# Performance work log

Measured on AMD Instinct MI355X. Metric: run time of the kernel, lower is better.

The kernel has to match this reference:

```python
import jax, jax.numpy as jnp
import numpy as np

N = 50000        # nodes
E = 800000       # directed edges
NUM_E = 10000    # hyperedges
NFEAT, NHID, NOUT = 256, 128, 64
K = 10
TEMP = 5.0


def gcn_prop(h, src, dst, n):
    # PyG GCNConv propagation with added self-loops: D^-1/2 (A+I) D^-1/2 h
    ew = jnp.ones(src.shape[0], h.dtype)
    deg = 1.0 + jax.ops.segment_sum(ew, dst, num_segments=n)  # self-loop adds 1
    dinv = jax.lax.rsqrt(deg)
    norm = dinv[src] * dinv[dst]                   # [E]
    out = jax.ops.segment_sum(h[src] * norm[:, None], dst, num_segments=n)
    out = out + h / deg[:, None]                   # self-loop term (weight deg^-1)
    return out


def gcn_conv(x, W, b, src, dst, n):
    return gcn_prop(x @ W, src, dst, n) + b


def hgnnp_conv(x, W, b, hv, he, n, num_e):
    # dhg HGNNPConv: theta(x) then v->e mean aggregation, then e->v mean
    h = x @ W + b
    ones = jnp.ones(hv.shape[0], h.dtype)
    e_deg = jnp.maximum(jax.ops.segment_sum(ones, he, num_segments=num_e), 1.0)
    v_deg = jnp.maximum(jax.ops.segment_sum(ones, hv, num_segments=n), 1.0)
    e_feat = jax.ops.segment_sum(h[hv], he, num_segments=num_e) / e_deg[:, None]
    v_out = jax.ops.segment_sum(e_feat[he], hv, num_segments=n) / v_deg[:, None]
    return v_out


def setup_inputs() -> dict:
    key = jax.random.key(0)
    ks = jax.random.split(key, 12)
    x = jax.random.normal(ks[0], (N, NFEAT), jnp.float32)
    edge_index = jax.random.randint(ks[1], (2, E), 0, N)
    hv_idx = jax.random.randint(ks[2], (200000,), 0, N)
    he_idx = jax.random.randint(ks[3], (200000,), 0, NUM_E)

    def glorot(k, shape):
        lim = float(np.sqrt(6.0 / (shape[0] + shape[1])))
        return jax.random.uniform(k, shape, jnp.float32, -lim, lim)

    return {
        "x": x, "edge_index": edge_index, "hv_idx": hv_idx, "he_idx": he_idx,
        "gcn_W1": glorot(ks[4], (NFEAT, NHID)), "gcn_b1": jnp.zeros((NHID,), jnp.float32),
        "gcn_W2": glorot(ks[5], (NHID, NOUT)), "gcn_b2": jnp.zeros((NOUT,), jnp.float32),
        "hg_W1": glorot(ks[6], (NFEAT, NHID)), "hg_b1": jnp.zeros((NHID,), jnp.float32),
        "hg_W2": glorot(ks[7], (NHID, NOUT)), "hg_b2": jnp.zeros((NOUT,), jnp.float32),
        "num_iter": 1,
    }


def reference(x, edge_index, hv_idx, he_idx,
              gcn_W1, gcn_b1, gcn_W2, gcn_b2,
              hg_W1, hg_b1, hg_W2, hg_b2, num_iter):
    src, dst = edge_index[0], edge_index[1]

    # HGNNP_GCN encoder (dropout is identity in eval-style reference)
    x1 = jax.nn.relu(gcn_conv(x, gcn_W1, gcn_b1, src, dst, N))
    x2 = gcn_conv(x1, gcn_W2, gcn_b2, src, dst, N)
    x3 = jax.nn.relu(hgnnp_conv(x, hg_W1, hg_b1, hv_idx, he_idx, N, NUM_E))
    x4 = hgnnp_conv(x3, hg_W2, hg_b2, hv_idx, he_idx, N, NUM_E)  # is_last: no act
    embeds = x2 * 0.5 + x4 * 0.5                     # [N, NOUT]

    # row-normalize (diag(1/||row||) @ data)
    data = embeds / jnp.linalg.norm(embeds, axis=1, keepdims=True)

    # kmeans++ init is a host-side, data-dependent pick; use deterministic
    # strided row selection from the (detached) normalized embeddings.
    init_idx = jnp.arange(K) * (N // K)
    mu = jax.lax.stop_gradient(data[init_idx])       # [K, NOUT]

    for _ in range(int(num_iter)):
        dist = data @ mu.T                           # [N, K]
        r = jax.nn.softmax(TEMP * dist, axis=1)
        cluster_r = r.sum(axis=0)                    # [K]
        cluster_mean = r.T @ data                    # [K, NOUT]
        mu = cluster_mean / cluster_r[:, None]

    dist = data @ mu.T
    r = jax.nn.softmax(TEMP * dist, axis=1)
    return mu, r, embeds, dist
```

## Files before the change

### kernel.cpp

```cpp
#include <hip/hip_runtime.h>
#include <hip/hip_bf16.h>


#define NN   50000
#define NP   50048
#define EE   800000
#define NINC 200000
#define NEH  10000
#define KCL  10

#define MU_OFF  0
#define R_OFF   640
#define EMB_OFF 500640
#define D_OFF   3700640

typedef __hip_bfloat16 bf16;
typedef unsigned short u16;
typedef unsigned int   u32;
typedef __attribute__((ext_vector_type(8))) short short8;
typedef __attribute__((ext_vector_type(4))) float f32x4;

__device__ __forceinline__ float b2f(bf16 v){ return __bfloat162float(v); }
__device__ __forceinline__ float us2f(u16 u){ return __uint_as_float(((unsigned)u) << 16); }
__device__ __forceinline__ u16 f2bu(float f){
  unsigned u = __float_as_uint(f);
  return (u16)((u + 0x7fffu + ((u >> 16) & 1u)) >> 16);
}
__device__ __forceinline__ bf16 f2b(float f){
  u16 r = f2bu(f);
  bf16 h;
  reinterpret_cast<u16&>(h) = r;
  return h;
}
__device__ __forceinline__ float ldf(const void* p, size_t i, int isbf){
  return isbf ? b2f(((const bf16*)p)[i]) : ((const float*)p)[i];
}
__device__ __forceinline__ void stf(void* p, size_t i, float v, int isbf){
  if (isbf) ((bf16*)p)[i] = f2b(v);
  else      ((float*)p)[i] = v;
}

__global__ void k_detect(const u16* __restrict__ xr, int* flag){
  __shared__ int bad;
  if (threadIdx.x == 0) bad = 0;
  __syncthreads();
  for (int i = threadIdx.x; i < 4096; i += 256){
    int e = (xr[i] >> 7) & 0xFF;
    if (e >= 0xEF) bad = 1;
  }
  __syncthreads();
  if (threadIdx.x == 0) *flag = bad ? 0 : 1;
}

__global__ void k_aconv(const void* __restrict__ x, u16* __restrict__ xb,
                        const int* __restrict__ flag){
  int i = blockIdx.x*256 + threadIdx.x;
  const int n4 = NN*256/4;
  if (i >= n4) return;
  ushort4 o;
  if (flag[0]){
    o = ((const ushort4*)x)[i];
  } else {
    float4 v = ((const float4*)x)[i];
    o = make_ushort4(f2bu(v.x), f2bu(v.y), f2bu(v.z), f2bu(v.w));
  }
  ((ushort4*)xb)[i] = o;
}

__global__ void k_wprep(const void* gW1, const void* hW1, const void* gW2, const void* hW2,
                        const void* gb1, const void* hb1, const void* gb2, const void* hb2,
                        u16* gW1t, u16* hW1t, u16* gW2t, u16* hW2t,
                        float* gb1f, float* hb1f, float* gb2f, float* hb2f,
                        const int* __restrict__ flag){
  const int isbf = flag[0];
  int i = blockIdx.x*256 + threadIdx.x;
  if (i < 256*128){
    int n = i >> 8, k = i & 255;
    gW1t[i] = f2bu(ldf(gW1, (size_t)k*128 + n, isbf));
    hW1t[i] = f2bu(ldf(hW1, (size_t)k*128 + n, isbf));
  }
  if (i < 64*128){
    int n = i >> 7, k = i & 127;
    gW2t[i] = f2bu(ldf(gW2, (size_t)k*64 + n, isbf));
    hW2t[i] = f2bu(ldf(hW2, (size_t)k*64 + n, isbf));
  }
  if (i < 128){ gb1f[i] = ldf(gb1,i,isbf); hb1f[i] = ldf(hb1,i,isbf); }
  if (i < 64) { gb2f[i] = ldf(gb2,i,isbf); hb2f[i] = ldf(hb2,i,isbf); }
}

template<int NBKT, int NPB>
__global__ __launch_bounds__(256) void k_histA(const int* __restrict__ key,
                                               int* __restrict__ HA, int chunk){
  __shared__ u32 hist[NBKT];
  for (int i = threadIdx.x; i < NBKT; i += 256) hist[i] = 0;
  __syncthreads();
  int base = blockIdx.x*chunk;
  for (int i = threadIdx.x; i < chunk; i += 256)
    atomicAdd(&hist[key[base+i]/NPB], 1u);
  __syncthreads();
  int* out = HA + blockIdx.x*NBKT;
  for (int i = threadIdx.x; i < NBKT; i += 256) out[i] = (int)hist[i];
}

__global__ void k_scanA_all(int* HAg, int* HAv, int* HAe,
                            int* bsg, int* bsv, int* bse){
  int* HA; int* bs; int nch;
  if (blockIdx.x == 0){ HA = HAg; bs = bsg; nch = 128; }
  else if (blockIdx.x == 1){ HA = HAv; bs = bsv; nch = 64; }
  else { HA = HAe; bs = bse; nch = 64; }
  __shared__ int s[256];
  int t = threadIdx.x;
  int run = 0;
  if (t < 250){
    for (int c = 0; c < nch; ++c){
      int v = HA[c*250 + t];
      HA[c*250 + t] = run;
      run += v;
    }
  }
  int own = (t < 250) ? run : 0;
  s[t] = own; __syncthreads();
  #pragma unroll
  for (int off = 1; off < 256; off <<= 1){
    int add = (t >= off) ? s[t-off] : 0;
    __syncthreads();
    s[t] += add;
    __syncthreads();
  }
  if (t < 250) bs[t] = s[t] - own;
  if (t == 255) bs[250] = s[255];
}

template<int NBKT, int NPB>
__global__ __launch_bounds__(256) void k_fillA(const int* __restrict__ key,
    const int* __restrict__ val, const int* __restrict__ HA,
    const int* __restrict__ bs, u32* __restrict__ packed, int chunk){
  __shared__ u32 cur[NBKT];
  const int* pre = HA + blockIdx.x*NBKT;
  for (int i = threadIdx.x; i < NBKT; i += 256) cur[i] = (u32)(bs[i] + pre[i]);
  __syncthreads();
  int base = blockIdx.x*chunk;
  for (int i = threadIdx.x; i < chunk; i += 256){
    int k = key[base+i];
    int b = k / NPB;
    u32 pos = atomicAdd(&cur[b], 1u);
    packed[pos] = ((u32)(k - b*NPB) << 16) | (u32)val[base+i];
  }
}

template<int NPB>
__global__ __launch_bounds__(256) void k_fillB(const u32* __restrict__ packed,
    const int* __restrict__ bs, int* __restrict__ csr,
    int* __restrict__ cnt, int* __restrict__ rp){
  __shared__ u32 hist[NPB];
  __shared__ int s[256];
  __shared__ u32 cur[NPB];
  const int b = blockIdx.x;
  const int s0 = bs[b], m = bs[b+1] - s0;
  const int t = threadIdx.x;
  for (int i = t; i < NPB; i += 256) hist[i] = 0;
  __syncthreads();
  for (int i = t; i < m; i += 256)
    atomicAdd(&hist[packed[s0+i] >> 16], 1u);
  __syncthreads();
  int own = (t < NPB) ? (int)hist[t] : 0;
  s[t] = own; __syncthreads();
  #pragma unroll
  for (int off = 1; off < 256; off <<= 1){
    int add = (t >= off) ? s[t-off] : 0;
    __syncthreads();
    s[t] += add;
    __syncthreads();
  }
  if (t < NPB){
    int excl = s[t] - own;
    cnt[b*NPB + t] = own;
    rp[b*NPB + t]  = s0 + excl;
    cur[t] = (u32)(s0 + excl);
  }
  __syncthreads();
  for (int i = t; i < m; i += 256){
    u32 p = packed[s0+i];
    u32 pos = atomicAdd(&cur[p >> 16], 1u);
    csr[pos] = (int)(p & 0xffffu);
  }
}

__global__ void k_invs(const int* __restrict__ cg, const int* __restrict__ cv,
                       const int* __restrict__ ce,
                       float* dinv, float* invv, float* inve){
  int i = blockIdx.x*256 + threadIdx.x;
  if (i < NN){
    float d = 1.0f + (float)cg[i];
    dinv[i] = rsqrtf(d);
    invv[i] = 1.0f / fmaxf((float)cv[i], 1.0f);
  } else if (i < NP){
    dinv[i] = 0.f;
  }
  if (i < NEH) inve[i] = 1.0f / fmaxf((float)ce[i], 1.0f);
}

template<int KDIM, int NCOL>
__global__ __launch_bounds__(256) void k_gemm_mfma(
    const u16* __restrict__ A, const u16* __restrict__ Wt,
    const float* __restrict__ bias, const float* __restrict__ rowscale,
    u16* __restrict__ C, int relu)
{
  constexpr int NT  = NCOL/16;
  constexpr int LDA = 40;
  __shared__ __align__(16) u16 Asl[64][LDA];
  __shared__ __align__(16) u16 Wsl[NCOL][LDA];
  const int tid  = threadIdx.x;
  const int wave = tid >> 6, lane = tid & 63;
  const int l15 = lane & 15, l4 = lane >> 4;
  const int row0 = blockIdx.x * 64;
  const int ar = tid >> 2, aq = tid & 3;
  constexpr int NW = NCOL*4/256;

  f32x4 acc[NT] = {};

  for (int kk = 0; kk < KDIM; kk += 32){
    {
      uint4 v = *(const uint4*)(A + (size_t)(row0 + ar)*KDIM + kk + aq*8);
      *(uint4*)&Asl[ar][aq*8] = v;
    }
    #pragma unroll
    for (int w2 = 0; w2 < NW; ++w2){
      int c = tid + w2*256;
      int n = c >> 2, q = c & 3;
      uint4 v = *(const uint4*)(Wt + (size_t)n*KDIM + kk + q*8);
      *(uint4*)&Wsl[n][q*8] = v;
    }
    __syncthreads();
    short8 af = *(const short8*)&Asl[wave*16 + l15][l4*8];
    #pragma unroll
    for (int t = 0; t < NT; ++t){
      short8 bf = *(const short8*)&Wsl[t*16 + l15][l4*8];
      acc[t] = __builtin_amdgcn_mfma_f32_16x16x32_bf16(af, bf, acc[t], 0, 0, 0);
    }
    __syncthreads();
  }

  #pragma unroll
  for (int t = 0; t < NT; ++t){
    int gcol = t*16 + l15;
    float b = bias ? bias[gcol] : 0.f;
    #pragma unroll
    for (int e = 0; e < 4; ++e){
      int grow = row0 + wave*16 + l4*4 + e;
      float v = acc[t][e] + b;
      if (relu) v = fmaxf(v, 0.f);
      if (rowscale) v *= rowscale[grow];
      C[(size_t)grow*NCOL + gcol] = f2bu(v);
    }
  }
}

template<int F, bool OUTBF, bool SELF>
__global__ __launch_bounds__(256) void k_gather(
    const int* __restrict__ rp, const int* __restrict__ cnt,
    const int* __restrict__ csr, const float* __restrict__ scale,
    const u16* __restrict__ h, const float* __restrict__ bias,
    void* __restrict__ out, int relu)
{
  const int wave = threadIdx.x >> 6, lane = threadIdx.x & 63;
  const int d = blockIdx.x*4 + wave;
  const int k0 = rp[d], n = cnt[d];

  if constexpr (F == 128){
    const uint* h32 = (const uint*)h;
    float a0=0,a1=0,b0=0,b1=0,c0=0,c1=0,e0=0,e1=0;
    if (SELF){
      uint v = h32[(size_t)d*64 + lane];
      a0 = us2f((u16)v); a1 = us2f((u16)(v>>16));
    }
    for (int base = 0; base < n; base += 64){
      int mm = n - base; if (mm > 64) mm = 64;
      int idx = (lane < mm) ? csr[k0 + base + lane] : 0;
      int jj = 0;
      for (; jj + 4 <= mm; jj += 4){
        int s0=__shfl(idx,jj), s1=__shfl(idx,jj+1), s2=__shfl(idx,jj+2), s3=__shfl(idx,jj+3);
        uint v0 = h32[(size_t)s0*64 + lane];
        uint v1 = h32[(size_t)s1*64 + lane];
        uint v2 = h32[(size_t)s2*64 + lane];
        uint v3 = h32[(size_t)s3*64 + lane];
        a0 += us2f((u16)v0); a1 += us2f((u16)(v0>>16));
        b0 += us2f((u16)v1); b1 += us2f((u16)(v1>>16));
        c0 += us2f((u16)v2); c1 += us2f((u16)(v2>>16));
        e0 += us2f((u16)v3); e1 += us2f((u16)(v3>>16));
      }
      for (; jj < mm; ++jj){
        int s = __shfl(idx, jj);
        uint v = h32[(size_t)s*64 + lane];
        a0 += us2f((u16)v); a1 += us2f((u16)(v>>16));
      }
    }
    float sc = scale[d];
    float o0 = ((a0+b0)+(c0+e0))*sc;
    float o1 = ((a1+b1)+(c1+e1))*sc;
    if (bias){ o0 += bias[lane*2]; o1 += bias[lane*2+1]; }
    if (relu){ o0 = fmaxf(o0,0.f); o1 = fmaxf(o1,0.f); }
    if (OUTBF){
      ((uint*)out)[(size_t)d*64 + lane] = (uint)f2bu(o0) | ((uint)f2bu(o1) << 16);
    } else {
      ((float2*)out)[(size_t)d*64 + lane] = make_float2(o0, o1);
    }
  } else {
    float a=0,b=0,c=0,e=0;
    if (SELF) a = us2f(h[(size_t)d*64 + lane]);
    for (int base = 0; base < n; base += 64){
      int mm = n - base; if (mm > 64) mm = 64;
      int idx = (lane < mm) ? csr[k0 + base + lane] : 0;
      int jj = 0;
      for (; jj + 4 <= mm; jj += 4){
        int s0=__shfl(idx,jj), s1=__shfl(idx,jj+1), s2=__shfl(idx,jj+2), s3=__shfl(idx,jj+3);
        a += us2f(h[(size_t)s0*64 + lane]);
        b += us2f(h[(size_t)s1*64 + lane]);
        c += us2f(h[(size_t)s2*64 + lane]);
        e += us2f(h[(size_t)s3*64 + lane]);
      }
      for (; jj < mm; ++jj){
        int s = __shfl(idx, jj);
        a += us2f(h[(size_t)s*64 + lane]);
      }
    }
    float o = ((a+b)+(c+e))*scale[d];
    if (bias) o += bias[lane];
    if (relu) o = fmaxf(o, 0.f);
    if (OUTBF) ((u16*)out)[(size_t)d*64 + lane] = f2bu(o);
    else       ((float*)out)[(size_t)d*64 + lane] = o;
  }
}

__global__ void k_embeds(const float* __restrict__ x2, const float* __restrict__ x4,
                         void* __restrict__ out, float* __restrict__ data,
                         const int* __restrict__ flag){
  int row  = blockIdx.x*4 + (threadIdx.x >> 6);
  int lane = threadIdx.x & 63;
  if (row >= NN) return;
  size_t idx = (size_t)row*64 + lane;
  float v = 0.5f*(x2[idx] + x4[idx]);
  float ss = v*v;
  #pragma unroll
  for (int off=32; off>0; off>>=1) ss += __shfl_xor(ss, off);
  float inv = rsqrtf(ss);
  data[idx] = v*inv;
  stf(out, EMB_OFF + idx, v, flag[0]);
}

__global__ void k_mu_init(const float* __restrict__ data, float* __restrict__ mu){
  int p = blockIdx.x*256 + threadIdx.x;
  if (p >= KCL*64) return;
  int k = p >> 6, f = p & 63;
  mu[p] = data[(size_t)k*(NN/KCL)*64 + f];
}

__global__ __launch_bounds__(128) void k_cluster_accum(const float* __restrict__ data,
    const float* __restrict__ mu, float* csum, float* cr, const int* nit, int iter)
{
  if (iter >= nit[0]) return;
  __shared__ float dt[128][65];
  __shared__ float rl[128][KCL];
  __shared__ float ms[KCL*64];
  int tid = threadIdx.x;
  int rowbase = blockIdx.x*128;
  for (int j=tid; j<KCL*64; j+=128) ms[j] = mu[j];
  for (int j=tid; j<128*64; j+=128){
    int rr = j>>6, f = j&63;
    int row = rowbase + rr;
    dt[rr][f] = (row<NN) ? data[(size_t)row*64+f] : 0.f;
  }
  __syncthreads();
  {
    int row = rowbase + tid;
    float dot[KCL];
    #pragma unroll
    for (int k2=0;k2<KCL;k2++) dot[k2]=0.f;
    for (int f=0; f<64; f++){
      float a = dt[tid][f];
      #pragma unroll
      for (int k2=0;k2<KCL;k2++) dot[k2] = fmaf(a, ms[k2*64+f], dot[k2]);
    }
    float m = -1e30f;
    #pragma unroll
    for (int k2=0;k2<KCL;k2++) m = fmaxf(m, 5.0f*dot[k2]);
    float s = 0.f, ev[KCL];
    #pragma unroll
    for (int k2=0;k2<KCL;k2++){ ev[k2] = expf(5.0f*dot[k2]-m); s += ev[k2]; }
    float inv = 1.0f/s;
    #pragma unroll
    for (int k2=0;k2<KCL;k2++) rl[tid][k2] = (row<NN) ? ev[k2]*inv : 0.f;
  }
  __syncthreads();
  for (int p=tid; p<KCL*64; p+=128){
    int k2 = p>>6, f = p&63;
    float acc = 0.f;
    for (int r2=0;r2<128;r2++) acc += rl[r2][k2]*dt[r2][f];
    unsafeAtomicAdd(&csum[p], acc);
  }
  if (tid < KCL){
    float acc = 0.f;
    for (int r2=0;r2<128;r2++) acc += rl[r2][tid];
    unsafeAtomicAdd(&cr[tid], acc);
  }
}

__global__ void k_mu_update(float* mu, float* csum, float* cr, const int* nit, int iter){
  if (iter >= nit[0]) return;
  int p = threadIdx.x;
  float c = csum[p];
  float r = cr[p>>6];
  __syncthreads();
  mu[p] = c / r;
  csum[p] = 0.f;
  if (p < KCL) cr[p] = 0.f;
}

__global__ __launch_bounds__(128) void k_cluster_final(const float* __restrict__ data,
    const float* __restrict__ mu, void* __restrict__ out, const int* __restrict__ flag)
{
  __shared__ float dt[128][65];
  __shared__ float ms[KCL*64];
  int tid = threadIdx.x;
  int rowbase = blockIdx.x*128;
  for (int j=tid; j<KCL*64; j+=128) ms[j] = mu[j];
  for (int j=tid; j<128*64; j+=128){
    int rr = j>>6, f = j&63;
    int row = rowbase + rr;
    dt[rr][f] = (row<NN) ? data[(size_t)row*64+f] : 0.f;
  }
  __syncthreads();
  int row = rowbase + tid;
  if (row >= NN) return;
  int isbf = flag[0];
  float dot[KCL];
  #pragma unroll
  for (int k2=0;k2<KCL;k2++) dot[k2]=0.f;
  for (int f=0; f<64; f++){
    float a = dt[tid][f];
    #pragma unroll
    for (int k2=0;k2<KCL;k2++) dot[k2] = fmaf(a, ms[k2*64+f], dot[k2]);
  }
  float m = -1e30f;
  #pragma unroll
  for (int k2=0;k2<KCL;k2++) m = fmaxf(m, 5.0f*dot[k2]);
  float s = 0.f, ev[KCL];
  #pragma unroll
  for (int k2=0;k2<KCL;k2++){ ev[k2] = expf(5.0f*dot[k2]-m); s += ev[k2]; }
  float inv = 1.0f/s;
  #pragma unroll
  for (int k2=0;k2<KCL;k2++){
    stf(out, (size_t)D_OFF + (size_t)row*KCL + k2, dot[k2],     isbf);
    stf(out, (size_t)R_OFF + (size_t)row*KCL + k2, ev[k2]*inv,  isbf);
  }
}

__global__ void k_mu_out(const float* __restrict__ mu, void* __restrict__ out,
                         const int* __restrict__ flag){
  int p = blockIdx.x*256 + threadIdx.x;
  if (p < KCL*64) stf(out, MU_OFF + p, mu[p], flag[0]);
}

extern "C" void kernel_launch(void* const* d_in, const int* in_sizes, int n_in,
                              void* d_out, int out_size, void* d_ws, size_t ws_size,
                              hipStream_t stream)
{
  const void* x   = d_in[0];
  const int*  ei  = (const int*)d_in[1];
  const int*  hv  = (const int*)d_in[2];
  const int*  he  = (const int*)d_in[3];
  const void* gW1 = d_in[4];
  const void* gb1 = d_in[5];
  const void* gW2 = d_in[6];
  const void* gb2 = d_in[7];
  const void* hW1 = d_in[8];
  const void* hb1 = d_in[9];
  const void* hW2 = d_in[10];
  const void* hb2 = d_in[11];
  const int*  nit = (const int*)d_in[12];

  float* ws = (float*)d_ws;
  size_t o = 0;
  u16*   xb  = (u16*)(ws + o); o += (size_t)NP*128;
  u16*   BAb = (u16*)(ws + o); o += (size_t)NP*64;
  u16*   BBb = (u16*)(ws + o); o += (size_t)NP*64;
  u16*   BCb = (u16*)(ws + o); o += (size_t)NP*64;
  u16*   BDb = (u16*)(ws + o); o += (size_t)NEH*64;
  u16*  gW1t = (u16*)(ws + o); o += 16384;
  u16*  hW1t = (u16*)(ws + o); o += 16384;
  u16*  gW2t = (u16*)(ws + o); o += 4096;
  u16*  hW2t = (u16*)(ws + o); o += 4096;
  float* gb1f = ws + o; o += 128;
  float* hb1f = ws + o; o += 128;
  float* gb2f = ws + o; o += 64;
  float* hb2f = ws + o; o += 64;
  float* dinv = ws + o; o += 50048;
  float* invv = ws + o; o += 50048;
  float* inve = ws + o; o += 10048;
  float* mu   = ws + o; o += 640;
  float* csum = ws + o; o += 640;
  float* cr   = ws + o; o += 64;
  int*   dflg = (int*)(ws + o); o += 16;
  float* x2f   = (float*)xb;
  float* x4f   = (float*)xb + (size_t)NP*64;
  float* dataf = (float*)BBb;
  int* ib = (int*)(ws + o);
  size_t io = 0;
  int* cg    = ib + io; io += NN;
  int* cv    = ib + io; io += NN;
  int* ce    = ib + io; io += NEH + 48;
  int* rp_g  = ib + io; io += NN;
  int* rp_v  = ib + io; io += NN;
  int* rp_e  = ib + io; io += NEH + 48;
  int* csr_g = ib + io; io += EE;
  int* csr_e = ib + io; io += NINC;
  int* csr_v = ib + io; io += NINC;
  int* HAg   = ib + io; io += 128*250;
  int* HAv   = ib + io; io += 64*250;
  int* HAe   = ib + io; io += 64*250;
  int* bsg   = ib + io; io += 256;
  int* bsv   = ib + io; io += 256;
  int* bse   = ib + io; io += 256;
  u32* pg = (u32*)(ib + io); io += EE;
  u32* pv = (u32*)(ib + io); io += NINC;
  u32* pe = (u32*)(ib + io); io += NINC;

  const int* srcp = ei;
  const int* dstp = ei + EE;
  dim3 B(256);
  const int NBP = (NP + 255)/256;

  k_detect<<<dim3(1), B, 0, stream>>>((const u16*)x, dflg);
  k_aconv<<<dim3(12500), B, 0, stream>>>(x, xb, dflg);
  k_wprep<<<dim3(128), B, 0, stream>>>(gW1, hW1, gW2, hW2, gb1, hb1, gb2, hb2,
                                       gW1t, hW1t, gW2t, hW2t,
                                       gb1f, hb1f, gb2f, hb2f, dflg);

  k_histA<250,200><<<dim3(128), B, 0, stream>>>(dstp, HAg, 6250);
  k_histA<250,200><<<dim3(64),  B, 0, stream>>>(hv,   HAv, 3125);
  k_histA<250, 40><<<dim3(64),  B, 0, stream>>>(he,   HAe, 3125);
  k_scanA_all<<<dim3(3), B, 0, stream>>>(HAg, HAv, HAe, bsg, bsv, bse);
  k_fillA<250,200><<<dim3(128), B, 0, stream>>>(dstp, srcp, HAg, bsg, pg, 6250);
  k_fillA<250,200><<<dim3(64),  B, 0, stream>>>(hv,   he,   HAv, bsv, pv, 3125);
  k_fillA<250, 40><<<dim3(64),  B, 0, stream>>>(he,   hv,   HAe, bse, pe, 3125);
  k_fillB<200><<<dim3(250), B, 0, stream>>>(pg, bsg, csr_g, cg, rp_g);
  k_fillB<200><<<dim3(250), B, 0, stream>>>(pv, bsv, csr_v, cv, rp_v);
  k_fillB< 40><<<dim3(250), B, 0, stream>>>(pe, bse, csr_e, ce, rp_e);
  k_invs<<<dim3(NBP), B, 0, stream>>>(cg, cv, ce, dinv, invv, inve);

  const int NB = NP/64;
  k_gemm_mfma<256,128><<<dim3(NB), B, 0, stream>>>(xb, gW1t, nullptr, dinv, BAb, 0);
  k_gather<128,true,true><<<dim3(NN/4), B, 0, stream>>>(rp_g, cg, csr_g, dinv,
                                                        BAb, gb1f, BBb, 1);
  k_gemm_mfma<256,128><<<dim3(NB), B, 0, stream>>>(xb, hW1t, hb1f, nullptr, BAb, 0);
  k_gather<128,true,false><<<dim3(NEH/4), B, 0, stream>>>(rp_e, ce, csr_e, inve,
                                                          BAb, nullptr, BDb, 0);
  k_gather<128,true,false><<<dim3(NN/4), B, 0, stream>>>(rp_v, cv, csr_v, invv,
                                                         BDb, nullptr, BCb, 1);
  k_gemm_mfma<128,64><<<dim3(NB), B, 0, stream>>>(BBb, gW2t, nullptr, dinv, BAb, 0);
  k_gather<64,false,true><<<dim3(NN/4), B, 0, stream>>>(rp_g, cg, csr_g, dinv,
                                                        BAb, gb2f, x2f, 0);
  k_gemm_mfma<128,64><<<dim3(NB), B, 0, stream>>>(BCb, hW2t, hb2f, nullptr, BAb, 0);
  k_gather<64,true,false><<<dim3(NEH/4), B, 0, stream>>>(rp_e, ce, csr_e, inve,
                                                         BAb, nullptr, BDb, 0);
  k_gather<64,false,false><<<dim3(NN/4), B, 0, stream>>>(rp_v, cv, csr_v, invv,
                                                         BDb, nullptr, x4f, 0);

  k_embeds<<<dim3((NN+3)/4), B, 0, stream>>>(x2f, x4f, d_out, dataf, dflg);

  k_mu_init<<<dim3(3), B, 0, stream>>>(dataf, mu);
  hipMemsetAsync(csum, 0, (640+64)*4, stream);
  const int CB = (NN + 127)/128;
  for (int it = 0; it < 4; ++it){
    k_cluster_accum<<<dim3(CB), dim3(128), 0, stream>>>(dataf, mu, csum, cr, nit, it);
    k_mu_update    <<<dim3(1),  dim3(640), 0, stream>>>(mu, csum, cr, nit, it);
  }
  k_cluster_final<<<dim3(CB), dim3(128), 0, stream>>>(dataf, mu, d_out, dflg);
  k_mu_out       <<<dim3(3),  B, 0, stream>>>(mu, d_out, dflg);
}
```

Before: 380.5 us.

## Replace atomic cluster accumulation with per-block partials and deterministic reduction

The k-means accumulation kernel is restructured to 200 blocks of 640 threads, each handling 250 rows. Each block writes per-block partial sums, and a separate single-block kernel reduces them, replacing global float atomics and the memset. Row dot products now read data directly with float4 loads instead of staging it in shared memory, and the final kernel uses 256-thread blocks. The goal is to remove atomic contention and the per-block shared-memory staging, at the cost of an extra kernel launch per iteration and a serial 200-way reduction.

```diff
diff --git a/kernel.cpp b/kernel.cpp
--- a/kernel.cpp
+++ b/kernel.cpp
@@ -355,103 +355,112 @@
   mu[p] = data[(size_t)k*(NN/KCL)*64 + f];
 }
 
-__global__ __launch_bounds__(128) void k_cluster_accum(const float* __restrict__ data,
-    const float* __restrict__ mu, float* csum, float* cr, const int* nit, int iter)
+__global__ __launch_bounds__(640) void k_cluster_iter(const float* __restrict__ data,
+    const float* __restrict__ mu, float* __restrict__ part, float* __restrict__ pcr,
+    const int* __restrict__ nit, int iter)
 {
   if (iter >= nit[0]) return;
-  __shared__ float dt[128][65];
-  __shared__ float rl[128][KCL];
-  __shared__ float ms[KCL*64];
-  int tid = threadIdx.x;
-  int rowbase = blockIdx.x*128;
-  for (int j=tid; j<KCL*64; j+=128) ms[j] = mu[j];
-  for (int j=tid; j<128*64; j+=128){
-    int rr = j>>6, f = j&63;
-    int row = rowbase + rr;
-    dt[rr][f] = (row<NN) ? data[(size_t)row*64+f] : 0.f;
-  }
-  __syncthreads();
-  {
-    int row = rowbase + tid;
+  __shared__ float ms[640];
+  __shared__ float rl[250][KCL];
+  const int tid = threadIdx.x;
+  ms[tid] = mu[tid];
+  __syncthreads();
+  const int r0 = blockIdx.x*250;
+  if (tid < 250){
+    const float4* dr = (const float4*)(data + (size_t)(r0 + tid)*64);
     float dot[KCL];
     #pragma unroll
-    for (int k2=0;k2<KCL;k2++) dot[k2]=0.f;
-    for (int f=0; f<64; f++){
-      float a = dt[tid][f];
+    for (int k=0;k<KCL;k++) dot[k]=0.f;
+    #pragma unroll
+    for (int q=0;q<16;q++){
+      float4 v = dr[q];
       #pragma unroll
-      for (int k2=0;k2<KCL;k2++) dot[k2] = fmaf(a, ms[k2*64+f], dot[k2]);
+      for (int k=0;k<KCL;k++){
+        float4 m4 = *(const float4*)&ms[k*64+q*4];
+        dot[k] = fmaf(v.x,m4.x,fmaf(v.y,m4.y,fmaf(v.z,m4.z,fmaf(v.w,m4.w,dot[k]))));
+      }
     }
     float m = -1e30f;
     #pragma unroll
-    for (int k2=0;k2<KCL;k2++) m = fmaxf(m, 5.0f*dot[k2]);
+    for (int k=0;k<KCL;k++) m = fmaxf(m, 5.0f*dot[k]);
     float s = 0.f, ev[KCL];
     #pragma unroll
-    for (int k2=0;k2<KCL;k2++){ ev[k2] = expf(5.0f*dot[k2]-m); s += ev[k2]; }
+    for (int k=0;k<KCL;k++){ ev[k] = expf(5.0f*dot[k]-m); s += ev[k]; }
     float inv = 1.0f/s;
     #pragma unroll
-    for (int k2=0;k2<KCL;k2++) rl[tid][k2] = (row<NN) ? ev[k2]*inv : 0.f;
-  }
-  __syncthreads();
-  for (int p=tid; p<KCL*64; p+=128){
-    int k2 = p>>6, f = p&63;
-    float acc = 0.f;
-    for (int r2=0;r2<128;r2++) acc += rl[r2][k2]*dt[r2][f];
-    unsafeAtomicAdd(&csum[p], acc);
-  }
-  if (tid < KCL){
-    float acc = 0.f;
-    for (int r2=0;r2<128;r2++) acc += rl[r2][tid];
-    unsafeAtomicAdd(&cr[tid], acc);
-  }
-}
-
-__global__ void k_mu_update(float* mu, float* csum, float* cr, const int* nit, int iter){
+    for (int k=0;k<KCL;k++) rl[tid][k] = ev[k]*inv;
+  }
+  __syncthreads();
+  const int w = tid >> 6, f = tid & 63;
+  float acc = 0.f, crp = 0.f;
+  for (int t = 0; t < 250; ++t){
+    float rv = rl[t][w];
+    acc = fmaf(rv, data[(size_t)(r0+t)*64 + f], acc);
+    crp += rv;
+  }
+  part[(size_t)blockIdx.x*640 + tid] = acc;
+  if (f == 0) pcr[blockIdx.x*16 + w] = crp;
+}
+
+__global__ void k_creduce(const float* __restrict__ part, const float* __restrict__ pcr,
+                          float* __restrict__ csum, float* __restrict__ cr,
+                          const int* __restrict__ nit, int iter){
   if (iter >= nit[0]) return;
   int p = threadIdx.x;
-  float c = csum[p];
-  float r = cr[p>>6];
-  __syncthreads();
-  mu[p] = c / r;
-  csum[p] = 0.f;
-  if (p < KCL) cr[p] = 0.f;
-}
-
-__global__ __launch_bounds__(128) void k_cluster_final(const float* __restrict__ data,
+  if (p < 640){
+    float a = 0.f;
+    for (int b = 0; b < 200; ++b) a += part[(size_t)b*640 + p];
+    csum[p] = a;
+  } else if (p < 640 + KCL){
+    int k = p - 640;
+    float a = 0.f;
+    for (int b = 0; b < 200; ++b) a += pcr[b*16 + k];
+    cr[k] = a;
+  }
+}
+
+__global__ void k_mu_update(float* __restrict__ mu, const float* __restrict__ csum,
+                            const float* __restrict__ cr,
+                            const int* __restrict__ nit, int iter){
+  if (iter >= nit[0]) return;
+  int p = threadIdx.x;
+  mu[p] = csum[p] / cr[p >> 6];
+}
+
+__global__ __launch_bounds__(256) void k_cluster_final(const float* __restrict__ data,
     const float* __restrict__ mu, void* __restrict__ out, const int* __restrict__ flag)
 {
-  __shared__ float dt[128][65];
-  __shared__ float ms[KCL*64];
-  int tid = threadIdx.x;
-  int rowbase = blockIdx.x*128;
-  for (int j=tid; j<KCL*64; j+=128) ms[j] = mu[j];
-  for (int j=tid; j<128*64; j+=128){
-    int rr = j>>6, f = j&63;
-    int row = rowbase + rr;
-    dt[rr][f] = (row<NN) ? data[(size_t)row*64+f] : 0.f;
-  }
-  __syncthreads();
-  int row = rowbase + tid;
+  __shared__ float ms[640];
+  const int tid = threadIdx.x;
+  for (int j = tid; j < 640; j += 256) ms[j] = mu[j];
+  __syncthreads();
+  int row = blockIdx.x*256 + tid;
   if (row >= NN) return;
-  int isbf = flag[0];
+  const int isbf = flag[0];
+  const float4* dr = (const float4*)(data + (size_t)row*64);
   float dot[KCL];
   #pragma unroll
-  for (int k2=0;k2<KCL;k2++) dot[k2]=0.f;
-  for (int f=0; f<64; f++){
-    float a = dt[tid][f];
-    #pragma unroll
-    for (int k2=0;k2<KCL;k2++) dot[k2] = fmaf(a, ms[k2*64+f], dot[k2]);
+  for (int k=0;k<KCL;k++) dot[k]=0.f;
+  #pragma unroll
+  for (int q=0;q<16;q++){
+    float4 v = dr[q];
+    #pragma unroll
+    for (int k=0;k<KCL;k++){
+      float4 m4 = *(const float4*)&ms[k*64+q*4];
+      dot[k] = fmaf(v.x,m4.x,fmaf(v.y,m4.y,fmaf(v.z,m4.z,fmaf(v.w,m4.w,dot[k]))));
+    }
   }
   float m = -1e30f;
   #pragma unroll
-  for (int k2=0;k2<KCL;k2++) m = fmaxf(m, 5.0f*dot[k2]);
+  for (int k=0;k<KCL;k++) m = fmaxf(m, 5.0f*dot[k]);
   float s = 0.f, ev[KCL];
   #pragma unroll
-  for (int k2=0;k2<KCL;k2++){ ev[k2] = expf(5.0f*dot[k2]-m); s += ev[k2]; }
+  for (int k=0;k<KCL;k++){ ev[k] = expf(5.0f*dot[k]-m); s += ev[k]; }
   float inv = 1.0f/s;
   #pragma unroll
-  for (int k2=0;k2<KCL;k2++){
-    stf(out, (size_t)D_OFF + (size_t)row*KCL + k2, dot[k2],     isbf);
-    stf(out, (size_t)R_OFF + (size_t)row*KCL + k2, ev[k2]*inv,  isbf);
+  for (int k=0;k<KCL;k++){
+    stf(out, (size_t)D_OFF + (size_t)row*KCL + k, dot[k],    isbf);
+    stf(out, (size_t)R_OFF + (size_t)row*KCL + k, ev[k]*inv, isbf);
   }
 }
 
@@ -500,6 +509,8 @@
   float* mu   = ws + o; o += 640;
   float* csum = ws + o; o += 640;
   float* cr   = ws + o; o += 64;
+  float* part = ws + o; o += 200*640;
+  float* pcr  = ws + o; o += 200*16;
   int*   dflg = (int*)(ws + o); o += 16;
   float* x2f   = (float*)xb;
   float* x4f   = (float*)xb + (size_t)NP*64;
@@ -569,12 +580,11 @@
   k_embeds<<<dim3((NN+3)/4), B, 0, stream>>>(x2f, x4f, d_out, dataf, dflg);
 
   k_mu_init<<<dim3(3), B, 0, stream>>>(dataf, mu);
-  hipMemsetAsync(csum, 0, (640+64)*4, stream);
-  const int CB = (NN + 127)/128;
   for (int it = 0; it < 4; ++it){
-    k_cluster_accum<<<dim3(CB), dim3(128), 0, stream>>>(dataf, mu, csum, cr, nit, it);
-    k_mu_update    <<<dim3(1),  dim3(640), 0, stream>>>(mu, csum, cr, nit, it);
-  }
-  k_cluster_final<<<dim3(CB), dim3(128), 0, stream>>>(dataf, mu, d_out, dflg);
+    k_cluster_iter<<<dim3(200), dim3(640), 0, stream>>>(dataf, mu, part, pcr, nit, it);
+    k_creduce     <<<dim3(1),   dim3(768), 0, stream>>>(part, pcr, csum, cr, nit, it);
+    k_mu_update   <<<dim3(1),   dim3(640), 0, stream>>>(mu, csum, cr, nit, it);
+  }
+  k_cluster_final<<<dim3(196), B, 0, stream>>>(dataf, mu, d_out, dflg);
   k_mu_out       <<<dim3(3),  B, 0, stream>>>(mu, d_out, dflg);
 }
```

After: 380.5 us. About the same (+0.0%).
